# Optimization experiments

Measured on AMD Instinct MI355X. Metric: run time of the kernel, lower is better.

The kernel has to match this reference:

```python
import jax, jax.numpy as jnp
import numpy as np

B, S, H, NH, HD = 4, 2048, 2048, 16, 128
SCALE = HD ** -0.5


def rotate_half(x):
    x1, x2 = jnp.split(x, 2, axis=-1)
    return jnp.concatenate([-x2, x1], axis=-1)


def setup_inputs() -> dict:
    key = jax.random.key(0)
    ks = jax.random.split(key, 8)
    x = jax.random.normal(ks[0], (B, S, H), dtype=jnp.float32)
    # RoPE tables for positions 0..S-1, standard theta=10000 construction
    inv_freq = 1.0 / (10000.0 ** (jnp.arange(0, HD, 2, dtype=jnp.float32) / HD))
    t = jnp.arange(S, dtype=jnp.float32)
    freqs = jnp.einsum('s,d->sd', t, inv_freq)          # [S, HD/2]
    emb = jnp.concatenate([freqs, freqs], axis=-1)      # [S, HD]
    cos, sin = jnp.cos(emb), jnp.sin(emb)
    # causal mask: True = masked (future positions)
    mask = jnp.triu(jnp.ones((S, S), dtype=bool), k=1)
    std = H ** -0.5
    Wq = jax.random.normal(ks[1], (H, H), dtype=jnp.float32) * std
    Wk = jax.random.normal(ks[2], (H, H), dtype=jnp.float32) * std
    Wv = jax.random.normal(ks[3], (H, H), dtype=jnp.float32) * std
    Wo = jax.random.normal(ks[4], (H, H), dtype=jnp.float32) * std
    return {"x": x, "cos": cos, "sin": sin, "mask": mask,
            "Wq": Wq, "Wk": Wk, "Wv": Wv, "Wo": Wo}


def reference(x, cos, sin, mask, Wq, Wk, Wv, Wo):
    # projections: nn.Linear(bias=False) => x @ W.T
    def proj(W):
        y = jnp.einsum('bsh,ih->bsi', x, W)             # [B,S,inner]
        return y.reshape(B, S, NH, HD).transpose(0, 2, 1, 3)  # [B,NH,S,HD]
    q, k, v = proj(Wq), proj(Wk), proj(Wv)
    # RoPE (rotate-half), cos/sin broadcast over batch & heads
    c = cos[None, None, :, :]
    s = sin[None, None, :, :]
    q = q * c + rotate_half(q) * s
    k = k * c + rotate_half(k) * s
    # attention
    attn = jnp.einsum('bhqd,bhkd->bhqk', q, k) * SCALE
    attn = jnp.where(mask[None, None, :, :], -jnp.inf, attn)
    attn = jax.nn.softmax(attn, axis=-1)
    out = jnp.einsum('bhqk,bhkd->bhqd', attn, v)
    out = out.transpose(0, 2, 1, 3).reshape(B, S, NH * HD)
    y = jnp.einsum('bsi,hi->bsh', out, Wo)
    return y, k, v
```

## Files before the change

kernel.cpp:

```cpp
#include <hip/hip_runtime.h>
#include <hip/hip_bf16.h>
#include <math.h>

typedef __bf16 bf16_t;
typedef __bf16 bf16x8 __attribute__((ext_vector_type(8)));
typedef __bf16 bf16x4v __attribute__((ext_vector_type(4)));
typedef float  f32x4  __attribute__((ext_vector_type(4)));
typedef float  f32x16 __attribute__((ext_vector_type(16)));
typedef unsigned int u32x4 __attribute__((ext_vector_type(4)));

constexpr int CB = 4, CS = 2048, CH = 2048, CNH = 16, CHD = 128;
constexpr int CM = CB * CS;
constexpr float CSCALE = 0.08838834764831845f;
constexpr float CL2E   = 1.4426950408889634f;
constexpr float CSC2   = CSCALE * CL2E;

__device__ __forceinline__ float fexp2(float x) {
  float r;
  asm("v_exp_f32 %0, %1" : "=v"(r) : "v"(x));
  return r;
}

__device__ __forceinline__ void g2l16(const void* g, void* l) {
  __builtin_amdgcn_global_load_lds(
      (const __attribute__((address_space(1))) void*)g,
      (__attribute__((address_space(3))) void*)l, 16, 0, 0);
}

__global__ __launch_bounds__(256) void cvt_kernel(const float* __restrict__ in,
                                                  bf16_t* __restrict__ out, int n4) {
  int i = blockIdx.x * 256 + threadIdx.x;
  if (i >= n4) return;
  float4 v = reinterpret_cast<const float4*>(in)[i];
  bf16x4v o = {(bf16_t)v.x, (bf16_t)v.y, (bf16_t)v.z, (bf16_t)v.w};
  reinterpret_cast<bf16x4v*>(out)[i] = o;
}

__device__ __forceinline__ void gemm256sq_core(const bf16_t* __restrict__ A,
                                               const bf16_t* __restrict__ Bm,
                                               bf16_t (*As2)[4][64 * 64],
                                               bf16_t (*Bs2)[4][64 * 64],
                                               int row0, int col0,
                                               f32x4 (&acc)[8][4]) {
  const int tid = threadIdx.x, lane = tid & 63, w = tid >> 6;
  const int wm = w >> 2, wn = w & 3;
  constexpr int NKT = CH / 64;
  const int id = w * 64 + lane;
  const int rl = id >> 3, ck = id & 7;

  auto stA = [&](int buf, int kt, int q) {
    const int row = q * 64 + rl;
    g2l16(A + (size_t)(row0 + row) * CH + kt * 64 + ((ck ^ (row & 7)) << 3),
          &As2[buf][q][id * 8]);
  };
  auto stB = [&](int buf, int kt, int q) {
    const int row = q * 64 + rl;
    g2l16(Bm + (size_t)(col0 + row) * CH + kt * 64 + ((ck ^ (row & 7)) << 3),
          &Bs2[buf][q][id * 8]);
  };
  auto rdA = [&](int buf, int r, int c) -> bf16x8 {
    return *(const bf16x8*)(&As2[buf][r >> 6][(r & 63) * 64 + ((c ^ (r & 7)) << 3)]);
  };
  auto rdB = [&](int buf, int r, int c) -> bf16x8 {
    return *(const bf16x8*)(&Bs2[buf][r >> 6][(r & 63) * 64 + ((c ^ (r & 7)) << 3)]);
  };

#pragma unroll
  for (int q = 0; q < 4; ++q) stB(0, 0, q);
#pragma unroll
  for (int q = 0; q < 4; ++q) stA(0, 0, q);
  asm volatile("s_waitcnt vmcnt(0)" ::: "memory");
  __builtin_amdgcn_s_barrier();
  __builtin_amdgcn_sched_barrier(0);

  const int ar0 = wm * 128 + (lane & 15);
  const int br0 = wn * 64 + (lane & 15);
  const int chi = lane >> 4;

  for (int t = 0; t < NKT; ++t) {
    const int buf = t & 1, nbuf = buf ^ 1;
    const bool pf = (t + 1 < NKT);
    bf16x8 bb[4][2], aa[2][2];

#pragma unroll
    for (int p = 0; p < 4; ++p) {
      if (p == 0) {
#pragma unroll
        for (int nf = 0; nf < 4; ++nf)
#pragma unroll
          for (int kk = 0; kk < 2; ++kk)
            bb[nf][kk] = rdB(buf, br0 + nf * 16, kk * 4 + chi);
      }
#pragma unroll
      for (int i = 0; i < 2; ++i)
#pragma unroll
        for (int kk = 0; kk < 2; ++kk)
          aa[i][kk] = rdA(buf, ar0 + (2 * p + i) * 16, kk * 4 + chi);

      if (pf) {
        if (p == 0) { stB(nbuf, t + 1, 0); stB(nbuf, t + 1, 1); }
        if (p == 1) { stB(nbuf, t + 1, 2); stB(nbuf, t + 1, 3); }
        if (p == 2) { stA(nbuf, t + 1, 0); stA(nbuf, t + 1, 2); }
        if (p == 3) { stA(nbuf, t + 1, 1); stA(nbuf, t + 1, 3); }
      }

      __builtin_amdgcn_s_barrier();
      asm volatile("s_waitcnt lgkmcnt(0)" ::: "memory");
      __builtin_amdgcn_sched_barrier(0);
      __builtin_amdgcn_s_setprio(1);
#pragma unroll
      for (int i = 0; i < 2; ++i)
#pragma unroll
        for (int nf = 0; nf < 4; ++nf)
#pragma unroll
          for (int kk = 0; kk < 2; ++kk)
            acc[2 * p + i][nf] = __builtin_amdgcn_mfma_f32_16x16x32_bf16(
                aa[i][kk], bb[nf][kk], acc[2 * p + i][nf], 0, 0, 0);
      __builtin_amdgcn_s_setprio(0);

      if (p == 1) {
        if (pf) { asm volatile("s_waitcnt vmcnt(4)" ::: "memory"); }
        else    { asm volatile("s_waitcnt vmcnt(0)" ::: "memory"); }
      }
      if (p == 3 && pf) { asm volatile("s_waitcnt vmcnt(2)" ::: "memory"); }
      __builtin_amdgcn_s_barrier();
      __builtin_amdgcn_sched_barrier(0);
    }
  }
}

__global__ __launch_bounds__(512, 1) void qkv_gemm(const bf16_t* __restrict__ xb,
                                                   const bf16_t* __restrict__ wqb,
                                                   const bf16_t* __restrict__ wkb,
                                                   const bf16_t* __restrict__ wvb,
                                                   bf16_t* __restrict__ qraw,
                                                   bf16_t* __restrict__ kraw,
                                                   bf16_t* __restrict__ vt,
                                                   float* __restrict__ vout) {
  __shared__ __align__(16) bf16_t As2[2][4][64 * 64];
  __shared__ __align__(16) bf16_t Bs2[2][4][64 * 64];
  const int z = blockIdx.z;
  const bf16_t* Bm = (z == 0) ? wqb : ((z == 1) ? wkb : wvb);
  const int row0 = blockIdx.x * 256, col0 = blockIdx.y * 256;
  f32x4 acc[8][4] = {};
  gemm256sq_core(xb, Bm, As2, Bs2, row0, col0, acc);

  const int lane = threadIdx.x & 63, w = threadIdx.x >> 6;
  const int wm = w >> 2, wn = w & 3;
#pragma unroll
  for (int i = 0; i < 8; ++i) {
#pragma unroll
    for (int j = 0; j < 4; ++j) {
      const int gr0 = row0 + wm * 128 + i * 16 + (lane >> 4) * 4;
      const int gc = col0 + wn * 64 + j * 16 + (lane & 15);
      const int b = gr0 >> 11, s0 = gr0 & (CS - 1);
      const int nh = gc >> 7, hd = gc & (CHD - 1);
      if (z == 2) {
#pragma unroll
        for (int r = 0; r < 4; ++r) {
          const size_t idx = ((size_t)(b * CNH + nh) * CS + s0 + r) * CHD + hd;
          vout[idx] = acc[i][j][r];
        }
        bf16x4v pv = {(bf16_t)acc[i][j][0], (bf16_t)acc[i][j][1],
                      (bf16_t)acc[i][j][2], (bf16_t)acc[i][j][3]};
        *(bf16x4v*)(vt + ((size_t)(b * CNH + nh) * CHD + hd) * CS + s0) = pv;
      } else {
        bf16_t* dst = (z == 0) ? qraw : kraw;
#pragma unroll
        for (int r = 0; r < 4; ++r) {
          const size_t idx = ((size_t)(b * CNH + nh) * CS + s0 + r) * CHD + hd;
          dst[idx] = (bf16_t)acc[i][j][r];
        }
      }
    }
  }
}

__global__ __launch_bounds__(512, 1) void y_gemm(const bf16_t* __restrict__ ob,
                                                 const bf16_t* __restrict__ wob,
                                                 float* __restrict__ yout) {
  __shared__ __align__(16) bf16_t As2[2][4][64 * 64];
  __shared__ __align__(16) bf16_t Bs2[2][4][64 * 64];
  const int row0 = blockIdx.x * 256, col0 = blockIdx.y * 256;
  f32x4 acc[8][4] = {};
  gemm256sq_core(ob, wob, As2, Bs2, row0, col0, acc);
  const int lane = threadIdx.x & 63, w = threadIdx.x >> 6;
  const int wm = w >> 2, wn = w & 3;
#pragma unroll
  for (int i = 0; i < 8; ++i)
#pragma unroll
    for (int j = 0; j < 4; ++j)
#pragma unroll
      for (int r = 0; r < 4; ++r) {
        const int gr = row0 + wm * 128 + i * 16 + (lane >> 4) * 4 + r;
        const int gc = col0 + wn * 64 + j * 16 + (lane & 15);
        yout[(size_t)gr * CH + gc] = acc[i][j][r];
      }
}

__global__ __launch_bounds__(256) void rope_kernel(bf16_t* __restrict__ qraw,
                                                   bf16_t* __restrict__ kraw,
                                                   const float* __restrict__ cosd,
                                                   const float* __restrict__ sind,
                                                   float* __restrict__ kout) {
  const int gid = blockIdx.x * 256 + threadIdx.x;
  const int isK = blockIdx.y;
  bf16_t* p = isK ? kraw : qraw;
  const int row = gid >> 3, d0 = (gid & 7) << 3;
  const int s = row & (CS - 1);
  const size_t base = (size_t)row * CHD;
  bf16x8 v1 = *(bf16x8*)(p + base + d0);
  bf16x8 v2 = *(bf16x8*)(p + base + d0 + 64);
  float c[8], sn[8];
  *(float4*)(c)      = *(const float4*)(cosd + s * CHD + d0);
  *(float4*)(c + 4)  = *(const float4*)(cosd + s * CHD + d0 + 4);
  *(float4*)(sn)     = *(const float4*)(sind + s * CHD + d0);
  *(float4*)(sn + 4) = *(const float4*)(sind + s * CHD + d0 + 4);
  float f1[8], f2[8];
  bf16x8 o1, o2;
#pragma unroll
  for (int i = 0; i < 8; ++i) {
    const float x1 = (float)v1[i], x2 = (float)v2[i];
    f1[i] = x1 * c[i] - x2 * sn[i];
    f2[i] = x2 * c[i] + x1 * sn[i];
    o1[i] = (bf16_t)f1[i];
    o2[i] = (bf16_t)f2[i];
  }
  *(bf16x8*)(p + base + d0) = o1;
  *(bf16x8*)(p + base + d0 + 64) = o2;
  if (isK) {
    *(float4*)(kout + base + d0)          = *(float4*)(f1);
    *(float4*)(kout + base + d0 + 4)      = *(float4*)(f1 + 4);
    *(float4*)(kout + base + d0 + 64)     = *(float4*)(f2);
    *(float4*)(kout + base + d0 + 64 + 4) = *(float4*)(f2 + 4);
  }
}

__global__ __launch_bounds__(256) void attn_kernel(const bf16_t* __restrict__ qb,
                                                   const bf16_t* __restrict__ kb,
                                                   const bf16_t* __restrict__ vt,
                                                   bf16_t* __restrict__ ob) {
  __shared__ __align__(16) bf16_t Ks[2][64 * 128];
  __shared__ __align__(16) bf16_t Vs[2][128 * 64];
  const int tid = threadIdx.x, lane = tid & 63, w = tid >> 6;
  const int hi = lane >> 5, l31 = lane & 31;

  const int swz = (blockIdx.x & 7) * 128 + (blockIdx.x >> 3);
  const int bh = swz >> 4;
  const int qt = 15 - (swz & 15);

  const int b = bh >> 4, nh = bh & (CNH - 1);
  const size_t kvbase_g = (size_t)bh * CS * CHD;
  const bf16_t* vbh = vt + (size_t)bh * CHD * CS;
  const int qw0 = qt * 128 + w * 32;
  const int qrow = qw0 + l31;

  bf16x8 bq[8];
  {
    const bf16_t* qp = qb + kvbase_g + (size_t)qrow * CHD + hi * 8;
#pragma unroll
    for (int ks = 0; ks < 8; ++ks) bq[ks] = *(const bf16x8*)(qp + ks * 16);
  }

  float m_ = -INFINITY, l_ = 0.f;
  f32x16 o_[4] = {};

  auto stage = [&](int buf, int kt) {
    const bf16_t* kbase = kb + kvbase_g + (size_t)kt * 64 * CHD;
#pragma unroll
    for (int i = 0; i < 4; ++i) {
      const int c = i * 256 + tid;
      const int r = c >> 4, ck = c & 15;
      g2l16(kbase + (size_t)r * CHD + ((ck ^ (r & 15)) << 3),
            &Ks[buf][(size_t)(i * 256 + (tid & ~63)) * 8 + (size_t)(lane) * 8]);
    }
#pragma unroll
    for (int i = 0; i < 4; ++i) {
      const int c = i * 256 + tid;
      const int r = c >> 3, ck = c & 7;
      g2l16(vbh + (size_t)r * CS + kt * 64 + ((ck ^ (r & 7)) << 3),
            &Vs[buf][(size_t)(i * 256 + (tid & ~63)) * 8 + (size_t)(lane) * 8]);
    }
  };

  const int nt = 2 * qt + 2;
  stage(0, 0);
  int cur = 0;

  for (int kt = 0; kt < nt; ++kt) {
    if (kt + 1 < nt) {
      stage(cur ^ 1, kt + 1);
      asm volatile("s_waitcnt vmcnt(8)" ::: "memory");
    } else {
      asm volatile("s_waitcnt vmcnt(0)" ::: "memory");
    }
    __builtin_amdgcn_s_barrier();
    __builtin_amdgcn_sched_barrier(0);

    f32x16 st[2] = {};
#pragma unroll
    for (int kb2 = 0; kb2 < 2; ++kb2) {
      const int krow = kb2 * 32 + l31;
#pragma unroll
      for (int ks = 0; ks < 8; ++ks) {
        const int c = (ks * 2 + hi) ^ (krow & 15);
        bf16x8 ak = *(const bf16x8*)(&Ks[cur][krow * 128 + (c << 3)]);
        st[kb2] = __builtin_amdgcn_mfma_f32_32x32x16_bf16(ak, bq[ks], st[kb2], 0, 0, 0);
      }
    }

    const int kvb = kt * 64;
    const bool anymask = (kvb + 63) > qw0;
#pragma unroll
    for (int blk = 0; blk < 2; ++blk)
#pragma unroll
      for (int r = 0; r < 16; ++r) {
        float xv = st[blk][r] * CSC2;
        if (anymask) {
          const int kv = kvb + blk * 32 + 4 * hi + (r & 3) + 8 * (r >> 2);
          if (kv > qrow) xv = -INFINITY;
        }
        st[blk][r] = xv;
      }

    float tmax = st[0][0];
#pragma unroll
    for (int r = 1; r < 16; ++r) tmax = fmaxf(tmax, st[0][r]);
#pragma unroll
    for (int r = 0; r < 16; ++r) tmax = fmaxf(tmax, st[1][r]);
    tmax = fmaxf(tmax, __shfl_xor(tmax, 32, 64));

    if (__any(tmax - m_ > 8.0f)) {
      const float mn = fmaxf(m_, tmax);
      const float corr = fexp2(m_ - mn);
      m_ = mn;
      l_ *= corr;
#pragma unroll
      for (int hb = 0; hb < 4; ++hb) o_[hb] *= corr;
    }

    f32x16 pe[2];
    float psum = 0.f;
#pragma unroll
    for (int blk = 0; blk < 2; ++blk)
#pragma unroll
      for (int r = 0; r < 16; ++r) {
        const float pv = fexp2(st[blk][r] - m_);
        pe[blk][r] = pv;
        psum += pv;
      }
    psum += __shfl_xor(psum, 32, 64);
    l_ += psum;

    bf16x8 pb[4];
#pragma unroll
    for (int ks = 0; ks < 4; ++ks) {
      const int blk = ks >> 1, r0 = (ks & 1) * 8;
      unsigned pw0, pw1, pw2, pw3;
      asm("v_cvt_pk_bf16_f32 %0, %1, %2" : "=v"(pw0) : "v"(pe[blk][r0 + 0]), "v"(pe[blk][r0 + 1]));
      asm("v_cvt_pk_bf16_f32 %0, %1, %2" : "=v"(pw2) : "v"(pe[blk][r0 + 4]), "v"(pe[blk][r0 + 5]));
      asm("v_cvt_pk_bf16_f32 %0, %1, %2" : "=v"(pw1) : "v"(pe[blk][r0 + 2]), "v"(pe[blk][r0 + 3]));
      asm("v_cvt_pk_bf16_f32 %0, %1, %2" : "=v"(pw3) : "v"(pe[blk][r0 + 6]), "v"(pe[blk][r0 + 7]));
      asm("v_permlane32_swap_b32 %0, %1" : "+v"(pw0), "+v"(pw2));
      asm("v_permlane32_swap_b32 %0, %1" : "+v"(pw1), "+v"(pw3));
      u32x4 pk = {pw0, pw1, pw2, pw3};
      pb[ks] = *reinterpret_cast<bf16x8*>(&pk);
    }

#pragma unroll
    for (int hb = 0; hb < 4; ++hb) {
      const int vrow = hb * 32 + l31;
#pragma unroll
      for (int ks = 0; ks < 4; ++ks) {
        const int c = (ks * 2 + hi) ^ (vrow & 7);
        bf16x8 av = *(const bf16x8*)(&Vs[cur][vrow * 64 + (c << 3)]);
        o_[hb] = __builtin_amdgcn_mfma_f32_32x32x16_bf16(av, pb[ks], o_[hb], 0, 0, 0);
      }
    }

    __builtin_amdgcn_s_barrier();
    __builtin_amdgcn_sched_barrier(0);
    cur ^= 1;
  }

  const float linv = 1.0f / l_;
  bf16_t* orow = ob + ((size_t)(b * CS + qrow)) * CH + nh * CHD;
#pragma unroll
  for (int hb = 0; hb < 4; ++hb)
#pragma unroll
    for (int g = 0; g < 4; ++g) {
      bf16x4v pv = {(bf16_t)(o_[hb][4 * g + 0] * linv), (bf16_t)(o_[hb][4 * g + 1] * linv),
                    (bf16_t)(o_[hb][4 * g + 2] * linv), (bf16_t)(o_[hb][4 * g + 3] * linv)};
      *(bf16x4v*)(orow + hb * 32 + 4 * hi + 8 * g) = pv;
    }
}

extern "C" void kernel_launch(void* const* d_in, const int* in_sizes, int n_in,
                              void* d_out, int out_size, void* d_ws, size_t ws_size,
                              hipStream_t stream) {
  const float* x    = (const float*)d_in[0];
  const float* cosd = (const float*)d_in[1];
  const float* sind = (const float*)d_in[2];
  const float* Wq = (const float*)d_in[4];
  const float* Wk = (const float*)d_in[5];
  const float* Wv = (const float*)d_in[6];
  const float* Wo = (const float*)d_in[7];

  float* yout = (float*)d_out;
  float* kout = yout + (size_t)CM * CH;
  float* vout = kout + (size_t)CM * CH;

  char* ws = (char*)d_ws;
  size_t off = 0;
  auto wsalloc = [&](size_t bytes) {
    void* p = ws + off;
    off += (bytes + 255) & ~(size_t)255;
    return p;
  };
  bf16_t* xb   = (bf16_t*)wsalloc((size_t)CM * CH * 2);
  bf16_t* wqb  = (bf16_t*)wsalloc((size_t)CH * CH * 2);
  bf16_t* wkb  = (bf16_t*)wsalloc((size_t)CH * CH * 2);
  bf16_t* wvb  = (bf16_t*)wsalloc((size_t)CH * CH * 2);
  bf16_t* wob  = (bf16_t*)wsalloc((size_t)CH * CH * 2);
  bf16_t* qraw = (bf16_t*)wsalloc((size_t)CM * CH * 2);
  bf16_t* kraw = (bf16_t*)wsalloc((size_t)CM * CH * 2);
  bf16_t* vt   = (bf16_t*)wsalloc((size_t)CM * CH * 2);
  bf16_t* ob   = (bf16_t*)wsalloc((size_t)CM * CH * 2);

  cvt_kernel<<<CM * CH / 4 / 256, 256, 0, stream>>>(x, xb, CM * CH / 4);
  cvt_kernel<<<CH * CH / 4 / 256, 256, 0, stream>>>(Wq, wqb, CH * CH / 4);
  cvt_kernel<<<CH * CH / 4 / 256, 256, 0, stream>>>(Wk, wkb, CH * CH / 4);
  cvt_kernel<<<CH * CH / 4 / 256, 256, 0, stream>>>(Wv, wvb, CH * CH / 4);
  cvt_kernel<<<CH * CH / 4 / 256, 256, 0, stream>>>(Wo, wob, CH * CH / 4);

  qkv_gemm<<<dim3(CM / 256, CH / 256, 3), 512, 0, stream>>>(xb, wqb, wkb, wvb,
                                                            qraw, kraw, vt, vout);
  rope_kernel<<<dim3(CB * CNH * CS * 8 / 256, 2), 256, 0, stream>>>(qraw, kraw, cosd,
                                                                    sind, kout);
  attn_kernel<<<CB * CNH * (CS / 128), 256, 0, stream>>>(qraw, kraw, vt, ob);
  y_gemm<<<dim3(CM / 256, CH / 256), 512, 0, stream>>>(ob, wob, yout);
}
```

Baseline: 551.4 us.

## Store K and V in MFMA-native panel layouts and read them directly from global

The QKV GEMM now writes K and V into 16-wide panel layouts that match the MFMA operand fragments, and RoPE is adapted to the K panel layout. The attention kernel drops its LDS staging, double buffering and barriers and loads K/V fragments straight from global memory, using 128-thread blocks over 64 query rows. This removes the shared-memory traffic and synchronisation, but each wave now fetches K/V from global or L2 on its own with no explicit prefetch, which can expose memory latency and raise cache traffic.

```diff
diff --git a/kernel.cpp b/kernel.cpp
--- a/kernel.cpp
+++ b/kernel.cpp
@@ -134,8 +134,8 @@
                                                    const bf16_t* __restrict__ wkb,
                                                    const bf16_t* __restrict__ wvb,
                                                    bf16_t* __restrict__ qraw,
-                                                   bf16_t* __restrict__ kraw,
-                                                   bf16_t* __restrict__ vt,
+                                                   bf16_t* __restrict__ knat,
+                                                   bf16_t* __restrict__ vt2,
                                                    float* __restrict__ vout) {
   __shared__ __align__(16) bf16_t As2[2][4][64 * 64];
   __shared__ __align__(16) bf16_t Bs2[2][4][64 * 64];
@@ -155,21 +155,26 @@
       const int gc = col0 + wn * 64 + j * 16 + (lane & 15);
       const int b = gr0 >> 11, s0 = gr0 & (CS - 1);
       const int nh = gc >> 7, hd = gc & (CHD - 1);
+      const int bh = b * CNH + nh;
       if (z == 2) {
 #pragma unroll
         for (int r = 0; r < 4; ++r) {
-          const size_t idx = ((size_t)(b * CNH + nh) * CS + s0 + r) * CHD + hd;
+          const size_t idx = ((size_t)bh * CS + s0 + r) * CHD + hd;
           vout[idx] = acc[i][j][r];
         }
         bf16x4v pv = {(bf16_t)acc[i][j][0], (bf16_t)acc[i][j][1],
                       (bf16_t)acc[i][j][2], (bf16_t)acc[i][j][3]};
-        *(bf16x4v*)(vt + ((size_t)(b * CNH + nh) * CHD + hd) * CS + s0) = pv;
+        *(bf16x4v*)(vt2 + (((size_t)bh * (CS / 16) + (s0 >> 4)) * CHD + hd) * 16 +
+                    (s0 & 15)) = pv;
+      } else if (z == 1) {
+        bf16_t* kp = knat + (((size_t)bh * 8 + (hd >> 4)) * CS + s0) * 16 + (hd & 15);
+#pragma unroll
+        for (int r = 0; r < 4; ++r) kp[r * 16] = (bf16_t)acc[i][j][r];
       } else {
-        bf16_t* dst = (z == 0) ? qraw : kraw;
 #pragma unroll
         for (int r = 0; r < 4; ++r) {
-          const size_t idx = ((size_t)(b * CNH + nh) * CS + s0 + r) * CHD + hd;
-          dst[idx] = (bf16_t)acc[i][j][r];
+          const size_t idx = ((size_t)bh * CS + s0 + r) * CHD + hd;
+          qraw[idx] = (bf16_t)acc[i][j][r];
         }
       }
     }
@@ -199,65 +204,86 @@
 }
 
 __global__ __launch_bounds__(256) void rope_kernel(bf16_t* __restrict__ qraw,
-                                                   bf16_t* __restrict__ kraw,
+                                                   bf16_t* __restrict__ knat,
                                                    const float* __restrict__ cosd,
                                                    const float* __restrict__ sind,
                                                    float* __restrict__ kout) {
   const int gid = blockIdx.x * 256 + threadIdx.x;
-  const int isK = blockIdx.y;
-  bf16_t* p = isK ? kraw : qraw;
-  const int row = gid >> 3, d0 = (gid & 7) << 3;
-  const int s = row & (CS - 1);
-  const size_t base = (size_t)row * CHD;
-  bf16x8 v1 = *(bf16x8*)(p + base + d0);
-  bf16x8 v2 = *(bf16x8*)(p + base + d0 + 64);
-  float c[8], sn[8];
-  *(float4*)(c)      = *(const float4*)(cosd + s * CHD + d0);
-  *(float4*)(c + 4)  = *(const float4*)(cosd + s * CHD + d0 + 4);
-  *(float4*)(sn)     = *(const float4*)(sind + s * CHD + d0);
-  *(float4*)(sn + 4) = *(const float4*)(sind + s * CHD + d0 + 4);
-  float f1[8], f2[8];
-  bf16x8 o1, o2;
-#pragma unroll
-  for (int i = 0; i < 8; ++i) {
-    const float x1 = (float)v1[i], x2 = (float)v2[i];
-    f1[i] = x1 * c[i] - x2 * sn[i];
-    f2[i] = x2 * c[i] + x1 * sn[i];
-    o1[i] = (bf16_t)f1[i];
-    o2[i] = (bf16_t)f2[i];
+  if (blockIdx.y == 0) {
+    bf16_t* p = qraw;
+    const int row = gid >> 3, d0 = (gid & 7) << 3;
+    const int s = row & (CS - 1);
+    const size_t base = (size_t)row * CHD;
+    bf16x8 v1 = *(bf16x8*)(p + base + d0);
+    bf16x8 v2 = *(bf16x8*)(p + base + d0 + 64);
+    float c[8], sn[8];
+    *(float4*)(c)      = *(const float4*)(cosd + s * CHD + d0);
+    *(float4*)(c + 4)  = *(const float4*)(cosd + s * CHD + d0 + 4);
+    *(float4*)(sn)     = *(const float4*)(sind + s * CHD + d0);
+    *(float4*)(sn + 4) = *(const float4*)(sind + s * CHD + d0 + 4);
+    bf16x8 o1, o2;
+#pragma unroll
+    for (int i = 0; i < 8; ++i) {
+      const float x1 = (float)v1[i], x2 = (float)v2[i];
+      o1[i] = (bf16_t)(x1 * c[i] - x2 * sn[i]);
+      o2[i] = (bf16_t)(x2 * c[i] + x1 * sn[i]);
+    }
+    *(bf16x8*)(p + base + d0) = o1;
+    *(bf16x8*)(p + base + d0 + 64) = o2;
+  } else {
+    const int row = gid >> 3, sub = gid & 7;
+    const int pan = sub >> 1, hf = (sub & 1) * 8;
+    const int bh = row >> 11, s = row & (CS - 1);
+    const int d0 = pan * 16 + hf;
+    bf16_t* k1 = knat + (((size_t)bh * 8 + pan) * CS + s) * 16 + hf;
+    bf16_t* k2 = knat + (((size_t)bh * 8 + pan + 4) * CS + s) * 16 + hf;
+    bf16x8 v1 = *(bf16x8*)k1;
+    bf16x8 v2 = *(bf16x8*)k2;
+    float c[8], sn[8];
+    *(float4*)(c)      = *(const float4*)(cosd + s * CHD + d0);
+    *(float4*)(c + 4)  = *(const float4*)(cosd + s * CHD + d0 + 4);
+    *(float4*)(sn)     = *(const float4*)(sind + s * CHD + d0);
+    *(float4*)(sn + 4) = *(const float4*)(sind + s * CHD + d0 + 4);
+    float f1[8], f2[8];
+    bf16x8 o1, o2;
+#pragma unroll
+    for (int i = 0; i < 8; ++i) {
+      const float x1 = (float)v1[i], x2 = (float)v2[i];
+      f1[i] = x1 * c[i] - x2 * sn[i];
+      f2[i] = x2 * c[i] + x1 * sn[i];
+      o1[i] = (bf16_t)f1[i];
+      o2[i] = (bf16_t)f2[i];
+    }
+    *(bf16x8*)k1 = o1;
+    *(bf16x8*)k2 = o2;
+    const size_t kb = (size_t)row * CHD + d0;
+    *(float4*)(kout + kb)          = *(float4*)(f1);
+    *(float4*)(kout + kb + 4)      = *(float4*)(f1 + 4);
+    *(float4*)(kout + kb + 64)     = *(float4*)(f2);
+    *(float4*)(kout + kb + 64 + 4) = *(float4*)(f2 + 4);
   }
-  *(bf16x8*)(p + base + d0) = o1;
-  *(bf16x8*)(p + base + d0 + 64) = o2;
-  if (isK) {
-    *(float4*)(kout + base + d0)          = *(float4*)(f1);
-    *(float4*)(kout + base + d0 + 4)      = *(float4*)(f1 + 4);
-    *(float4*)(kout + base + d0 + 64)     = *(float4*)(f2);
-    *(float4*)(kout + base + d0 + 64 + 4) = *(float4*)(f2 + 4);
-  }
-}
-
-__global__ __launch_bounds__(256) void attn_kernel(const bf16_t* __restrict__ qb,
-                                                   const bf16_t* __restrict__ kb,
-                                                   const bf16_t* __restrict__ vt,
+}
+
+__global__ __launch_bounds__(128) void attn_kernel(const bf16_t* __restrict__ qb,
+                                                   const bf16_t* __restrict__ kn,
+                                                   const bf16_t* __restrict__ v2,
                                                    bf16_t* __restrict__ ob) {
-  __shared__ __align__(16) bf16_t Ks[2][64 * 128];
-  __shared__ __align__(16) bf16_t Vs[2][128 * 64];
   const int tid = threadIdx.x, lane = tid & 63, w = tid >> 6;
   const int hi = lane >> 5, l31 = lane & 31;
 
-  const int swz = (blockIdx.x & 7) * 128 + (blockIdx.x >> 3);
-  const int bh = swz >> 4;
-  const int qt = 15 - (swz & 15);
+  const int swz = (blockIdx.x & 7) * 256 + (blockIdx.x >> 3);
+  const int bh = swz >> 5;
+  const int qt = (31 - (swz & 31)) * 2 + w;
 
   const int b = bh >> 4, nh = bh & (CNH - 1);
-  const size_t kvbase_g = (size_t)bh * CS * CHD;
-  const bf16_t* vbh = vt + (size_t)bh * CHD * CS;
-  const int qw0 = qt * 128 + w * 32;
+  const bf16_t* kbase = kn + (size_t)bh * 8 * CS * 16;
+  const bf16_t* vbase = v2 + (size_t)bh * (CS / 16) * CHD * 16;
+  const int qw0 = qt * 32;
   const int qrow = qw0 + l31;
 
   bf16x8 bq[8];
   {
-    const bf16_t* qp = qb + kvbase_g + (size_t)qrow * CHD + hi * 8;
+    const bf16_t* qp = qb + ((size_t)bh * CS + qrow) * CHD + hi * 8;
 #pragma unroll
     for (int ks = 0; ks < 8; ++ks) bq[ks] = *(const bf16x8*)(qp + ks * 16);
   }
@@ -265,51 +291,21 @@
   float m_ = -INFINITY, l_ = 0.f;
   f32x16 o_[4] = {};
 
-  auto stage = [&](int buf, int kt) {
-    const bf16_t* kbase = kb + kvbase_g + (size_t)kt * 64 * CHD;
-#pragma unroll
-    for (int i = 0; i < 4; ++i) {
-      const int c = i * 256 + tid;
-      const int r = c >> 4, ck = c & 15;
-      g2l16(kbase + (size_t)r * CHD + ((ck ^ (r & 15)) << 3),
-            &Ks[buf][(size_t)(i * 256 + (tid & ~63)) * 8 + (size_t)(lane) * 8]);
-    }
-#pragma unroll
-    for (int i = 0; i < 4; ++i) {
-      const int c = i * 256 + tid;
-      const int r = c >> 3, ck = c & 7;
-      g2l16(vbh + (size_t)r * CS + kt * 64 + ((ck ^ (r & 7)) << 3),
-            &Vs[buf][(size_t)(i * 256 + (tid & ~63)) * 8 + (size_t)(lane) * 8]);
-    }
-  };
-
-  const int nt = 2 * qt + 2;
-  stage(0, 0);
-  int cur = 0;
-
+  const int nt = (qt >> 1) + 1;
   for (int kt = 0; kt < nt; ++kt) {
-    if (kt + 1 < nt) {
-      stage(cur ^ 1, kt + 1);
-      asm volatile("s_waitcnt vmcnt(8)" ::: "memory");
-    } else {
-      asm volatile("s_waitcnt vmcnt(0)" ::: "memory");
-    }
-    __builtin_amdgcn_s_barrier();
-    __builtin_amdgcn_sched_barrier(0);
+    const int kvb = kt * 64;
 
     f32x16 st[2] = {};
 #pragma unroll
     for (int kb2 = 0; kb2 < 2; ++kb2) {
-      const int krow = kb2 * 32 + l31;
+      const bf16_t* kr = kbase + (size_t)(kvb + kb2 * 32 + l31) * 16 + hi * 8;
 #pragma unroll
       for (int ks = 0; ks < 8; ++ks) {
-        const int c = (ks * 2 + hi) ^ (krow & 15);
-        bf16x8 ak = *(const bf16x8*)(&Ks[cur][krow * 128 + (c << 3)]);
+        bf16x8 ak = *(const bf16x8*)(kr + (size_t)ks * CS * 16);
         st[kb2] = __builtin_amdgcn_mfma_f32_32x32x16_bf16(ak, bq[ks], st[kb2], 0, 0, 0);
       }
     }
 
-    const int kvb = kt * 64;
     const bool anymask = (kvb + 63) > qw0;
 #pragma unroll
     for (int blk = 0; blk < 2; ++blk)
@@ -339,14 +335,13 @@
       for (int hb = 0; hb < 4; ++hb) o_[hb] *= corr;
     }
 
-    f32x16 pe[2];
     float psum = 0.f;
 #pragma unroll
     for (int blk = 0; blk < 2; ++blk)
 #pragma unroll
       for (int r = 0; r < 16; ++r) {
         const float pv = fexp2(st[blk][r] - m_);
-        pe[blk][r] = pv;
+        st[blk][r] = pv;
         psum += pv;
       }
     psum += __shfl_xor(psum, 32, 64);
@@ -357,10 +352,10 @@
     for (int ks = 0; ks < 4; ++ks) {
       const int blk = ks >> 1, r0 = (ks & 1) * 8;
       unsigned pw0, pw1, pw2, pw3;
-      asm("v_cvt_pk_bf16_f32 %0, %1, %2" : "=v"(pw0) : "v"(pe[blk][r0 + 0]), "v"(pe[blk][r0 + 1]));
-      asm("v_cvt_pk_bf16_f32 %0, %1, %2" : "=v"(pw2) : "v"(pe[blk][r0 + 4]), "v"(pe[blk][r0 + 5]));
-      asm("v_cvt_pk_bf16_f32 %0, %1, %2" : "=v"(pw1) : "v"(pe[blk][r0 + 2]), "v"(pe[blk][r0 + 3]));
-      asm("v_cvt_pk_bf16_f32 %0, %1, %2" : "=v"(pw3) : "v"(pe[blk][r0 + 6]), "v"(pe[blk][r0 + 7]));
+      asm("v_cvt_pk_bf16_f32 %0, %1, %2" : "=v"(pw0) : "v"(st[blk][r0 + 0]), "v"(st[blk][r0 + 1]));
+      asm("v_cvt_pk_bf16_f32 %0, %1, %2" : "=v"(pw2) : "v"(st[blk][r0 + 4]), "v"(st[blk][r0 + 5]));
+      asm("v_cvt_pk_bf16_f32 %0, %1, %2" : "=v"(pw1) : "v"(st[blk][r0 + 2]), "v"(st[blk][r0 + 3]));
+      asm("v_cvt_pk_bf16_f32 %0, %1, %2" : "=v"(pw3) : "v"(st[blk][r0 + 6]), "v"(st[blk][r0 + 7]));
       asm("v_permlane32_swap_b32 %0, %1" : "+v"(pw0), "+v"(pw2));
       asm("v_permlane32_swap_b32 %0, %1" : "+v"(pw1), "+v"(pw3));
       u32x4 pk = {pw0, pw1, pw2, pw3};
@@ -369,18 +364,13 @@
 
 #pragma unroll
     for (int hb = 0; hb < 4; ++hb) {
-      const int vrow = hb * 32 + l31;
+      const bf16_t* vr = vbase + ((size_t)(kvb >> 4) * CHD + hb * 32 + l31) * 16 + hi * 8;
 #pragma unroll
       for (int ks = 0; ks < 4; ++ks) {
-        const int c = (ks * 2 + hi) ^ (vrow & 7);
-        bf16x8 av = *(const bf16x8*)(&Vs[cur][vrow * 64 + (c << 3)]);
+        bf16x8 av = *(const bf16x8*)(vr + (size_t)ks * CHD * 16);
         o_[hb] = __builtin_amdgcn_mfma_f32_32x32x16_bf16(av, pb[ks], o_[hb], 0, 0, 0);
       }
     }
-
-    __builtin_amdgcn_s_barrier();
-    __builtin_amdgcn_sched_barrier(0);
-    cur ^= 1;
   }
 
   const float linv = 1.0f / l_;
@@ -423,8 +413,8 @@
   bf16_t* wvb  = (bf16_t*)wsalloc((size_t)CH * CH * 2);
   bf16_t* wob  = (bf16_t*)wsalloc((size_t)CH * CH * 2);
   bf16_t* qraw = (bf16_t*)wsalloc((size_t)CM * CH * 2);
-  bf16_t* kraw = (bf16_t*)wsalloc((size_t)CM * CH * 2);
-  bf16_t* vt   = (bf16_t*)wsalloc((size_t)CM * CH * 2);
+  bf16_t* knat = (bf16_t*)wsalloc((size_t)CM * CH * 2);
+  bf16_t* vt2  = (bf16_t*)wsalloc((size_t)CM * CH * 2);
   bf16_t* ob   = (bf16_t*)wsalloc((size_t)CM * CH * 2);
 
   cvt_kernel<<<CM * CH / 4 / 256, 256, 0, stream>>>(x, xb, CM * CH / 4);
@@ -434,9 +424,9 @@
   cvt_kernel<<<CH * CH / 4 / 256, 256, 0, stream>>>(Wo, wob, CH * CH / 4);
 
   qkv_gemm<<<dim3(CM / 256, CH / 256, 3), 512, 0, stream>>>(xb, wqb, wkb, wvb,
-                                                            qraw, kraw, vt, vout);
-  rope_kernel<<<dim3(CB * CNH * CS * 8 / 256, 2), 256, 0, stream>>>(qraw, kraw, cosd,
+                                                            qraw, knat, vt2, vout);
+  rope_kernel<<<dim3(CB * CNH * CS * 8 / 256, 2), 256, 0, stream>>>(qraw, knat, cosd,
                                                                     sind, kout);
-  attn_kernel<<<CB * CNH * (CS / 128), 256, 0, stream>>>(qraw, kraw, vt, ob);
+  attn_kernel<<<CB * CNH * (CS / 64), 128, 0, stream>>>(qraw, knat, vt2, ob);
   y_gemm<<<dim3(CM / 256, CH / 256), 512, 0, stream>>>(ob, wob, yout);
 }
```

Result: faster. 532.3 us (-3.5%).
